# Kernel optimization log

Measured on AMD Instinct MI355X. Metric: run time of the kernel, lower is better.

## Reference

```python
import jax, jax.numpy as jnp
import numpy as np

N = 6144          # num utterances (graph nodes)
D = 128           # utt_embed_size
WIN = 10          # att_window_size
NUM_SPK = 8
N_EMO = 7


def _init(key, shape):
    fan_in = shape[0]
    return jax.random.normal(key, shape, dtype=jnp.float32) * (1.0 / np.sqrt(fan_in))


def setup_inputs() -> dict:
    key = jax.random.key(0)
    ks = jax.random.split(key, 20)
    inp = {
        "x": jax.random.normal(ks[0], (N, D), dtype=jnp.float32),
        "speakers": jax.random.randint(ks[1], (N,), 0, NUM_SPK, dtype=jnp.int32),
        # layer-1 relation GCN weights (pred / suc / same / diff)
        "W_pred1": _init(ks[2], (D, D)),
        "W_suc1": _init(ks[3], (D, D)),
        "W_same1": _init(ks[4], (D, D)),
        "W_diff1": _init(ks[5], (D, D)),
        # layer-2 relation GCN weights
        "W_pred2": _init(ks[6], (D, D)),
        "W_suc2": _init(ks[7], (D, D)),
        "W_same2": _init(ks[8], (D, D)),
        "W_diff2": _init(ks[9], (D, D)),
        "w_aggr_1": _init(ks[10], (D, D)),
        "w_aggr_2": _init(ks[11], (D, D)),
        "w_e1": _init(ks[12], (2 * D, D)),
        "b_e1": jnp.zeros((D,), dtype=jnp.float32),
        "w_e2": _init(ks[13], (D, N_EMO)),
        "b_e2": jnp.zeros((N_EMO,), dtype=jnp.float32),
        "w_s": _init(ks[14], (2 * D, N_EMO)),
        "b_s": jnp.zeros((N_EMO,), dtype=jnp.float32),
    }
    return inp


def reference(x, speakers, W_pred1, W_suc1, W_same1, W_diff1,
              W_pred2, W_suc2, W_same2, W_diff2,
              w_aggr_1, w_aggr_2, w_e1, b_e1, w_e2, b_e2, w_s, b_s):
    n = x.shape[0]
    idx = jnp.arange(n)
    # windowed dot-product attention; entries outside the window stay 0.0
    # BEFORE the softmax (faithful to the torch code: zeros, not -inf)
    band = jnp.abs(idx[:, None] - idx[None, :]) <= WIN
    scores = jnp.where(band, x @ x.T, 0.0)            # [N, N]
    attn = jax.nn.softmax(scores, axis=1)
    # relation masks
    same = (speakers[:, None] == speakers[None, :]).astype(x.dtype)
    pred = (idx[None, :] >= idx[:, None]).astype(x.dtype)   # triu incl diag
    suc = 1.0 - pred                                          # strict lower tri
    adjs = (same * pred * attn,        # same-speaker, predecessor
            same * suc * attn,         # same-speaker, successor
            (1.0 - same) * pred * attn,  # diff-speaker, predecessor
            (1.0 - same) * suc * attn)   # diff-speaker, successor

    def gcn(h, Ws):  # sum_k adj_k @ (h @ W_k)
        return sum(a @ (h @ w) for a, w in zip(adjs, Ws))

    d = jnp.diagonal(attn)[:, None]   # self-attention scale
    h1 = jax.nn.relu(gcn(x, (W_pred1, W_suc1, W_same1, W_diff1))
                     + (x @ w_aggr_1) * d)
    h2 = jax.nn.relu(gcn(h1, (W_pred2, W_suc2, W_same2, W_diff2))
                     + (h1 @ w_aggr_2) * d)
    h = jnp.concatenate([h2, x], axis=1)              # [N, 2D]
    emotion = jax.nn.relu(h @ w_e1 + b_e1) @ w_e2 + b_e2   # [N, 7]
    sentiment = h @ w_s + b_s                               # [N, 7]
    return emotion, sentiment
```

## Files before the change

kernel.cpp:

```cpp
#include <hip/hip_runtime.h>
#include <hip/hip_bf16.h>


#define NN   6144
#define DD   128
#define WINW 10
#define YST  168

typedef unsigned short u16;
typedef __attribute__((ext_vector_type(8))) short bf16x8;
typedef __attribute__((ext_vector_type(4))) float f32x4;

__device__ __forceinline__ float b2f(u16 u) {
    return __uint_as_float(((unsigned int)u) << 16);
}
__device__ __forceinline__ u16 f2b(float f) {
    __hip_bfloat16 h = __float2bfloat16(f);
    return *reinterpret_cast<u16*>(&h);
}
__device__ __forceinline__ bf16x8 cvt8(const float* p) {
    float4 u = *reinterpret_cast<const float4*>(p);
    float4 v = *reinterpret_cast<const float4*>(p + 4);
    bf16x8 r;
    r[0] = (short)f2b(u.x); r[1] = (short)f2b(u.y);
    r[2] = (short)f2b(u.z); r[3] = (short)f2b(u.w);
    r[4] = (short)f2b(v.x); r[5] = (short)f2b(v.y);
    r[6] = (short)f2b(v.z); r[7] = (short)f2b(v.w);
    return r;
}

__global__ __launch_bounds__(256) void prep_kernel(
    const float* __restrict__ x,
    const float* __restrict__ p0, const float* __restrict__ p1,
    const float* __restrict__ p2, const float* __restrict__ p3,
    const float* __restrict__ p4,
    const float* __restrict__ q0, const float* __restrict__ q1,
    const float* __restrict__ q2, const float* __restrict__ q3,
    const float* __restrict__ q4,
    const float* __restrict__ we1, const float* __restrict__ we2,
    const float* __restrict__ ws,
    u16* __restrict__ W1T, u16* __restrict__ W2T, u16* __restrict__ We1T,
    u16* __restrict__ we2T, u16* __restrict__ wsT,
    float* __restrict__ bandw)
{
    const int tid = threadIdx.x;

    if (blockIdx.x < 64) {
        int t = blockIdx.x * 256 + tid;
        const float* Ws1[5] = {p0, p1, p2, p3, p4};
        const float* Ws2[5] = {q0, q1, q2, q3, q4};
        #pragma unroll
        for (int r = 0; r < 5; ++r) {
            int idx = t + r * 16384;
            int k = idx & 127, c = (idx >> 7) & 127;
            W1T[idx] = f2b(Ws1[r][k * 128 + c]);
            W2T[idx] = f2b(Ws2[r][k * 128 + c]);
        }
        #pragma unroll
        for (int r = 0; r < 2; ++r) {
            int idx = t + r * 16384;
            int n = idx >> 8, k = idx & 255;
            We1T[idx] = f2b(we1[k * 128 + n]);
        }
        if (blockIdx.x == 0) {
            #pragma unroll
            for (int r = 0; r < 8; ++r) {
                int idx = tid + r * 256;
                int n = idx >> 7, k = idx & 127;
                we2T[idx] = f2b(n < 7 ? we2[k * 7 + n] : 0.f);
            }
            #pragma unroll
            for (int r = 0; r < 16; ++r) {
                int idx = tid + r * 256;
                int n = idx >> 8, k = idx & 255;
                wsT[idx] = f2b(n < 7 ? ws[k * 7 + n] : 0.f);
            }
        }
        return;
    }

    __shared__ float Xs[52][132];
    __shared__ float Ss[32][24];
    const int r0 = (blockIdx.x - 64) * 32;

    #pragma unroll
    for (int it = 0; it < 7; ++it) {
        int f = tid + it * 256;
        if (f < 52 * 32) {
            int s = f >> 5, c = f & 31;
            int g = r0 - WINW + s;
            if (g >= 0 && g < NN)
                *reinterpret_cast<float4*>(&Xs[s][c * 4]) =
                    *reinterpret_cast<const float4*>(&x[(size_t)g * DD + c * 4]);
        }
    }
    __syncthreads();

    #pragma unroll
    for (int r = 0; r < 3; ++r) {
        int p = tid + r * 256;
        if (p >= 672) break;
        int il = p / 21, o = p - il * 21;
        int jg = r0 + il - WINW + o;
        float sv = -1e30f;
        if (jg >= 0 && jg < NN) {
            const float* xr = &Xs[il + WINW][0];
            const float* jr = &Xs[il + o][0];
            float a0 = 0.f, a1 = 0.f, a2 = 0.f, a3 = 0.f;
            #pragma unroll 8
            for (int k4 = 0; k4 < 32; ++k4) {
                float4 a = *reinterpret_cast<const float4*>(xr + k4 * 4);
                float4 b = *reinterpret_cast<const float4*>(jr + k4 * 4);
                a0 = fmaf(a.x, b.x, a0); a1 = fmaf(a.y, b.y, a1);
                a2 = fmaf(a.z, b.z, a2); a3 = fmaf(a.w, b.w, a3);
            }
            sv = (a0 + a1) + (a2 + a3);
        }
        Ss[il][o] = sv;
    }
    __syncthreads();

    if (tid < 32) {
        int il = tid, i = r0 + il;
        float m = 0.f;
        #pragma unroll
        for (int o = 0; o < 21; ++o) {
            float s = Ss[il][o];
            if (s > -1e29f) m = fmaxf(m, s);
        }
        int lo = i - WINW; if (lo < 0) lo = 0;
        int hi = i + WINW; if (hi > NN - 1) hi = NN - 1;
        float Z = (float)(NN - (hi - lo + 1)) * expf(-m);
        float ev[21];
        #pragma unroll
        for (int o = 0; o < 21; ++o) {
            float s = Ss[il][o];
            ev[o] = (s > -1e29f) ? expf(s - m) : 0.f;
            Z += ev[o];
        }
        #pragma unroll
        for (int o = 0; o < 21; ++o) bandw[i * 32 + o] = ev[o] / Z;
    }
}

__global__ __launch_bounds__(256) void layer_kernel(
    const float* __restrict__ Af, const u16* __restrict__ Ab16,
    const u16* __restrict__ BT, const float* __restrict__ bandw,
    const int* __restrict__ spk, u16* __restrict__ hout, int a_is_f32)
{
    __shared__ u16 Ys[52][YST];
    __shared__ int2 tab[32 * 22];
    const int tid  = threadIdx.x;
    const int wave = tid >> 6, lane = tid & 63;
    const int lm = lane & 15, quad = lane >> 4;
    const int wm = wave >> 1, wn = wave & 1;
    const int bm = blockIdx.y * 32;
    const int hb = blockIdx.x;

    for (int p = tid; p < 704; p += 256) {
        int il = p / 22, e = p - il * 22;
        int i  = bm + il;
        int si = spk[i];
        float w; int off;
        if (e < 21) {
            int j = i - WINW + e;
            bool valid = (j >= 0) && (j < NN);
            int jc  = valid ? j : i;
            int sel = (spk[jc] == si) ? ((j >= i) ? 0 : 1) : ((j >= i) ? 2 : 3);
            w   = valid ? bandw[(size_t)i * 32 + e] : 0.f;
            off = valid ? (il + e) * YST + sel * 32 : 0;
        } else {
            w   = bandw[(size_t)i * 32 + WINW];
            off = (il + WINW) * YST + 4 * 32;
        }
        tab[p] = make_int2(__float_as_int(w), off);
    }

    bf16x8 afr[2][4];
    #pragma unroll
    for (int mt = 0; mt < 2; ++mt) {
        int gr = bm - WINW + (wm * 2 + mt) * 16 + lm;
        gr = min(max(gr, 0), NN - 1);
        #pragma unroll
        for (int s = 0; s < 4; ++s) {
            if (a_is_f32)
                afr[mt][s] = cvt8(Af + (size_t)gr * DD + s * 32 + quad * 8);
            else
                afr[mt][s] = *reinterpret_cast<const bf16x8*>(
                    Ab16 + (size_t)gr * DD + s * 32 + quad * 8);
        }
    }

    f32x4 acc[2][5];
    #pragma unroll
    for (int mt = 0; mt < 2; ++mt)
        #pragma unroll
        for (int n = 0; n < 5; ++n) acc[mt][n] = {0.f, 0.f, 0.f, 0.f};

    #pragma unroll
    for (int np = 0; np < 5; ++np) {
        int nt = wn * 5 + np;
        int gn = (nt >> 1) * 128 + hb * 32 + (nt & 1) * 16 + lm;
        #pragma unroll
        for (int s = 0; s < 4; ++s) {
            bf16x8 b = *reinterpret_cast<const bf16x8*>(
                BT + (size_t)gn * DD + s * 32 + quad * 8);
            acc[0][np] = __builtin_amdgcn_mfma_f32_16x16x32_bf16(afr[0][s], b, acc[0][np], 0, 0, 0);
            acc[1][np] = __builtin_amdgcn_mfma_f32_16x16x32_bf16(afr[1][s], b, acc[1][np], 0, 0, 0);
        }
    }
    #pragma unroll
    for (int mt = 0; mt < 2; ++mt)
        #pragma unroll
        for (int np = 0; np < 5; ++np) {
            int nt = wn * 5 + np;
            #pragma unroll
            for (int r = 0; r < 4; ++r) {
                int lr = (wm * 2 + mt) * 16 + quad * 4 + r;
                if (lr < 52) Ys[lr][nt * 16 + lm] = f2b(acc[mt][np][r]);
            }
        }
    __syncthreads();

    const int c0 = (tid & 15) * 2;
    const int rg = tid >> 4;
    #pragma unroll
    for (int rr = 0; rr < 2; ++rr) {
        int il = rg * 2 + rr;
        float a0 = 0.f, a1 = 0.f;
        const int2* tp = &tab[il * 22];
        #pragma unroll
        for (int e = 0; e < 22; ++e) {
            int2 t = tp[e];
            float w = __int_as_float(t.x);
            unsigned y2 = *reinterpret_cast<const unsigned*>(
                &Ys[0][0] + t.y + c0);
            a0 = fmaf(w, b2f((u16)(y2 & 0xffff)), a0);
            a1 = fmaf(w, b2f((u16)(y2 >> 16)), a1);
        }
        int i = bm + il;
        unsigned pk = ((unsigned)f2b(fmaxf(a1, 0.f)) << 16) | f2b(fmaxf(a0, 0.f));
        *reinterpret_cast<unsigned*>(&hout[(size_t)i * DD + hb * 32 + c0]) = pk;
    }
}

__global__ __launch_bounds__(64) void head_kernel(
    const u16* __restrict__ h2b, const float* __restrict__ x,
    const u16* __restrict__ We1T, const float* __restrict__ be1,
    const u16* __restrict__ we2T, const float* __restrict__ be2,
    const u16* __restrict__ wsT,  const float* __restrict__ bs,
    float* __restrict__ out)
{
    __shared__ float Es[16][132];
    const int lane = threadIdx.x;
    const int lm = lane & 15, quad = lane >> 4;
    const int bm = blockIdx.x * 16;
    const int row = bm + lm;

    bf16x8 afr[8];
    #pragma unroll
    for (int s = 0; s < 4; ++s)
        afr[s] = *reinterpret_cast<const bf16x8*>(
            &h2b[(size_t)row * DD + s * 32 + quad * 8]);
    #pragma unroll
    for (int s = 4; s < 8; ++s)
        afr[s] = cvt8(&x[(size_t)row * DD + (s - 4) * 32 + quad * 8]);

    f32x4 accE[8], accS = {0.f, 0.f, 0.f, 0.f};
    #pragma unroll
    for (int nt = 0; nt < 8; ++nt) accE[nt] = {0.f, 0.f, 0.f, 0.f};

    #pragma unroll
    for (int s = 0; s < 8; ++s) {
        #pragma unroll
        for (int nt = 0; nt < 8; ++nt) {
            bf16x8 b = *reinterpret_cast<const bf16x8*>(
                &We1T[(size_t)(nt * 16 + lm) * 256 + s * 32 + quad * 8]);
            accE[nt] = __builtin_amdgcn_mfma_f32_16x16x32_bf16(afr[s], b, accE[nt], 0, 0, 0);
        }
        bf16x8 bsf = *reinterpret_cast<const bf16x8*>(
            &wsT[(size_t)lm * 256 + s * 32 + quad * 8]);
        accS = __builtin_amdgcn_mfma_f32_16x16x32_bf16(afr[s], bsf, accS, 0, 0, 0);
    }

    if (lm < 7) {
        #pragma unroll
        for (int r = 0; r < 4; ++r) {
            int i = bm + quad * 4 + r;
            out[(size_t)NN * 7 + (size_t)i * 7 + lm] = accS[r] + bs[lm];
        }
    }
    #pragma unroll
    for (int nt = 0; nt < 8; ++nt) {
        int col = nt * 16 + lm;
        float bias = be1[col];
        #pragma unroll
        for (int r = 0; r < 4; ++r)
            Es[quad * 4 + r][col] = fmaxf(accE[nt][r] + bias, 0.f);
    }
    __syncthreads();

    f32x4 accM = {0.f, 0.f, 0.f, 0.f};
    #pragma unroll
    for (int s = 0; s < 4; ++s) {
        bf16x8 a = cvt8(&Es[lm][s * 32 + quad * 8]);
        bf16x8 b = *reinterpret_cast<const bf16x8*>(
            &we2T[(size_t)lm * 128 + s * 32 + quad * 8]);
        accM = __builtin_amdgcn_mfma_f32_16x16x32_bf16(a, b, accM, 0, 0, 0);
    }
    if (lm < 7) {
        #pragma unroll
        for (int r = 0; r < 4; ++r) {
            int i = bm + quad * 4 + r;
            out[(size_t)i * 7 + lm] = accM[r] + be2[lm];
        }
    }
}

extern "C" void kernel_launch(void* const* d_in, const int* in_sizes, int n_in,
                              void* d_out, int out_size, void* d_ws, size_t ws_size,
                              hipStream_t stream)
{
    const float* x   = (const float*)d_in[0];
    const int*   spk = (const int*)d_in[1];
    const float* Wp1 = (const float*)d_in[2];
    const float* Wu1 = (const float*)d_in[3];
    const float* Wm1 = (const float*)d_in[4];
    const float* Wd1 = (const float*)d_in[5];
    const float* Wp2 = (const float*)d_in[6];
    const float* Wu2 = (const float*)d_in[7];
    const float* Wm2 = (const float*)d_in[8];
    const float* Wd2 = (const float*)d_in[9];
    const float* wa1 = (const float*)d_in[10];
    const float* wa2 = (const float*)d_in[11];
    const float* we1 = (const float*)d_in[12];
    const float* be1 = (const float*)d_in[13];
    const float* we2 = (const float*)d_in[14];
    const float* be2 = (const float*)d_in[15];
    const float* wss = (const float*)d_in[16];
    const float* bss = (const float*)d_in[17];

    char* base = (char*)d_ws;
    float* bandw = (float*)(base);
    u16*   W1T   = (u16*)(base + 786432);
    u16*   W2T   = (u16*)(base + 950272);
    u16*   We1T  = (u16*)(base + 1114112);
    u16*   we2T  = (u16*)(base + 1179648);
    u16*   wsT   = (u16*)(base + 1183744);
    u16*   h1b   = (u16*)(base + 1191936);
    u16*   h2b   = (u16*)(base + 2764800);

    prep_kernel<<<256, 256, 0, stream>>>(x, Wp1, Wu1, Wm1, Wd1, wa1,
                                         Wp2, Wu2, Wm2, Wd2, wa2,
                                         we1, we2, wss,
                                         W1T, W2T, We1T, we2T, wsT, bandw);
    layer_kernel<<<dim3(4, 192), 256, 0, stream>>>(x, nullptr, W1T, bandw, spk, h1b, 1);
    layer_kernel<<<dim3(4, 192), 256, 0, stream>>>(nullptr, h1b, W2T, bandw, spk, h2b, 0);
    head_kernel<<<384, 64, 0, stream>>>(h2b, x, We1T, be1, we2T, be2, wsT, bss,
                                        (float*)d_out);
}
```

Baseline: 139.2 us.

## Increase block counts across prep, layer and head kernels for more parallelism

The attention-score blocks in the prep kernel now cover 16 rows instead of 32, so that section launches twice as many blocks. The layer kernel's column slice shrinks from 32 to 16 output columns, giving eight blocks per row tile, and each wave now owns one 16-row M tile. The head kernel uses 4 waves per block, splitting the E1 output tiles across waves and handing the sentiment and second-layer MFMAs to single waves. The goal is to fill more CUs on a small problem. The cost is recomputing the A fragments, the halo rows and the neighbour table in more blocks, plus idle waves in the head's tail.

Measured after the change: 158.5 us. +13.8%, slower.

```diff
diff --git a/kernel.cpp b/kernel.cpp
--- a/kernel.cpp
+++ b/kernel.cpp
@@ -5,7 +5,7 @@
 #define NN   6144
 #define DD   128
 #define WINW 10
-#define YST  168
+#define YST  88
 
 typedef unsigned short u16;
 typedef __attribute__((ext_vector_type(8))) short bf16x8;
@@ -79,14 +79,14 @@
         return;
     }
 
-    __shared__ float Xs[52][132];
-    __shared__ float Ss[32][24];
-    const int r0 = (blockIdx.x - 64) * 32;
-
-    #pragma unroll
-    for (int it = 0; it < 7; ++it) {
+    __shared__ float Xs[36][132];
+    __shared__ float Ss[16][24];
+    const int r0 = (blockIdx.x - 64) * 16;
+
+    #pragma unroll
+    for (int it = 0; it < 5; ++it) {
         int f = tid + it * 256;
-        if (f < 52 * 32) {
+        if (f < 36 * 32) {
             int s = f >> 5, c = f & 31;
             int g = r0 - WINW + s;
             if (g >= 0 && g < NN)
@@ -97,9 +97,9 @@
     __syncthreads();
 
     #pragma unroll
-    for (int r = 0; r < 3; ++r) {
+    for (int r = 0; r < 2; ++r) {
         int p = tid + r * 256;
-        if (p >= 672) break;
+        if (p >= 336) break;
         int il = p / 21, o = p - il * 21;
         int jg = r0 + il - WINW + o;
         float sv = -1e30f;
@@ -120,7 +120,7 @@
     }
     __syncthreads();
 
-    if (tid < 32) {
+    if (tid < 16) {
         int il = tid, i = r0 + il;
         float m = 0.f;
         #pragma unroll
@@ -153,7 +153,6 @@
     const int tid  = threadIdx.x;
     const int wave = tid >> 6, lane = tid & 63;
     const int lm = lane & 15, quad = lane >> 4;
-    const int wm = wave >> 1, wn = wave & 1;
     const int bm = blockIdx.y * 32;
     const int hb = blockIdx.x;
 
@@ -168,83 +167,67 @@
             int jc  = valid ? j : i;
             int sel = (spk[jc] == si) ? ((j >= i) ? 0 : 1) : ((j >= i) ? 2 : 3);
             w   = valid ? bandw[(size_t)i * 32 + e] : 0.f;
-            off = valid ? (il + e) * YST + sel * 32 : 0;
+            off = valid ? (il + e) * YST + sel * 16 : 0;
         } else {
             w   = bandw[(size_t)i * 32 + WINW];
-            off = (il + WINW) * YST + 4 * 32;
+            off = (il + WINW) * YST + 4 * 16;
         }
         tab[p] = make_int2(__float_as_int(w), off);
     }
 
-    bf16x8 afr[2][4];
-    #pragma unroll
-    for (int mt = 0; mt < 2; ++mt) {
-        int gr = bm - WINW + (wm * 2 + mt) * 16 + lm;
-        gr = min(max(gr, 0), NN - 1);
-        #pragma unroll
-        for (int s = 0; s < 4; ++s) {
-            if (a_is_f32)
-                afr[mt][s] = cvt8(Af + (size_t)gr * DD + s * 32 + quad * 8);
-            else
-                afr[mt][s] = *reinterpret_cast<const bf16x8*>(
-                    Ab16 + (size_t)gr * DD + s * 32 + quad * 8);
-        }
-    }
-
-    f32x4 acc[2][5];
-    #pragma unroll
-    for (int mt = 0; mt < 2; ++mt)
-        #pragma unroll
-        for (int n = 0; n < 5; ++n) acc[mt][n] = {0.f, 0.f, 0.f, 0.f};
-
-    #pragma unroll
-    for (int np = 0; np < 5; ++np) {
-        int nt = wn * 5 + np;
-        int gn = (nt >> 1) * 128 + hb * 32 + (nt & 1) * 16 + lm;
+    int gr = bm - WINW + wave * 16 + lm;
+    gr = min(max(gr, 0), NN - 1);
+    bf16x8 afr[4];
+    #pragma unroll
+    for (int s = 0; s < 4; ++s) {
+        if (a_is_f32)
+            afr[s] = cvt8(Af + (size_t)gr * DD + s * 32 + quad * 8);
+        else
+            afr[s] = *reinterpret_cast<const bf16x8*>(
+                Ab16 + (size_t)gr * DD + s * 32 + quad * 8);
+    }
+
+    f32x4 acc[5];
+    #pragma unroll
+    for (int n = 0; n < 5; ++n) acc[n] = {0.f, 0.f, 0.f, 0.f};
+
+    #pragma unroll
+    for (int nt = 0; nt < 5; ++nt) {
+        int gn = nt * 128 + hb * 16 + lm;
         #pragma unroll
         for (int s = 0; s < 4; ++s) {
             bf16x8 b = *reinterpret_cast<const bf16x8*>(
                 BT + (size_t)gn * DD + s * 32 + quad * 8);
-            acc[0][np] = __builtin_amdgcn_mfma_f32_16x16x32_bf16(afr[0][s], b, acc[0][np], 0, 0, 0);
-            acc[1][np] = __builtin_amdgcn_mfma_f32_16x16x32_bf16(afr[1][s], b, acc[1][np], 0, 0, 0);
-        }
-    }
-    #pragma unroll
-    for (int mt = 0; mt < 2; ++mt)
-        #pragma unroll
-        for (int np = 0; np < 5; ++np) {
-            int nt = wn * 5 + np;
-            #pragma unroll
-            for (int r = 0; r < 4; ++r) {
-                int lr = (wm * 2 + mt) * 16 + quad * 4 + r;
-                if (lr < 52) Ys[lr][nt * 16 + lm] = f2b(acc[mt][np][r]);
-            }
+            acc[nt] = __builtin_amdgcn_mfma_f32_16x16x32_bf16(afr[s], b, acc[nt], 0, 0, 0);
+        }
+    }
+    #pragma unroll
+    for (int nt = 0; nt < 5; ++nt)
+        #pragma unroll
+        for (int r = 0; r < 4; ++r) {
+            int lr = wave * 16 + quad * 4 + r;
+            if (lr < 52) Ys[lr][nt * 16 + lm] = f2b(acc[nt][r]);
         }
     __syncthreads();
 
-    const int c0 = (tid & 15) * 2;
-    const int rg = tid >> 4;
-    #pragma unroll
-    for (int rr = 0; rr < 2; ++rr) {
-        int il = rg * 2 + rr;
-        float a0 = 0.f, a1 = 0.f;
-        const int2* tp = &tab[il * 22];
-        #pragma unroll
-        for (int e = 0; e < 22; ++e) {
-            int2 t = tp[e];
-            float w = __int_as_float(t.x);
-            unsigned y2 = *reinterpret_cast<const unsigned*>(
-                &Ys[0][0] + t.y + c0);
-            a0 = fmaf(w, b2f((u16)(y2 & 0xffff)), a0);
-            a1 = fmaf(w, b2f((u16)(y2 >> 16)), a1);
-        }
-        int i = bm + il;
-        unsigned pk = ((unsigned)f2b(fmaxf(a1, 0.f)) << 16) | f2b(fmaxf(a0, 0.f));
-        *reinterpret_cast<unsigned*>(&hout[(size_t)i * DD + hb * 32 + c0]) = pk;
-    }
-}
-
-__global__ __launch_bounds__(64) void head_kernel(
+    const int c0 = (tid & 7) * 2;
+    const int il = tid >> 3;
+    float a0 = 0.f, a1 = 0.f;
+    const int2* tp = &tab[il * 22];
+    #pragma unroll
+    for (int e = 0; e < 22; ++e) {
+        int2 t = tp[e];
+        float w = __int_as_float(t.x);
+        unsigned y2 = *reinterpret_cast<const unsigned*>(&Ys[0][0] + t.y + c0);
+        a0 = fmaf(w, b2f((u16)(y2 & 0xffff)), a0);
+        a1 = fmaf(w, b2f((u16)(y2 >> 16)), a1);
+    }
+    int i = bm + il;
+    unsigned pk = ((unsigned)f2b(fmaxf(a1, 0.f)) << 16) | f2b(fmaxf(a0, 0.f));
+    *reinterpret_cast<unsigned*>(&hout[(size_t)i * DD + hb * 16 + c0]) = pk;
+}
+
+__global__ __launch_bounds__(256) void head_kernel(
     const u16* __restrict__ h2b, const float* __restrict__ x,
     const u16* __restrict__ We1T, const float* __restrict__ be1,
     const u16* __restrict__ we2T, const float* __restrict__ be2,
@@ -252,7 +235,8 @@
     float* __restrict__ out)
 {
     __shared__ float Es[16][132];
-    const int lane = threadIdx.x;
+    const int tid  = threadIdx.x;
+    const int wave = tid >> 6, lane = tid & 63;
     const int lm = lane & 15, quad = lane >> 4;
     const int bm = blockIdx.x * 16;
     const int row = bm + lm;
@@ -266,24 +250,27 @@
     for (int s = 4; s < 8; ++s)
         afr[s] = cvt8(&x[(size_t)row * DD + (s - 4) * 32 + quad * 8]);
 
-    f32x4 accE[8], accS = {0.f, 0.f, 0.f, 0.f};
-    #pragma unroll
-    for (int nt = 0; nt < 8; ++nt) accE[nt] = {0.f, 0.f, 0.f, 0.f};
+    f32x4 accE[2], accS = {0.f, 0.f, 0.f, 0.f};
+    accE[0] = {0.f, 0.f, 0.f, 0.f};
+    accE[1] = {0.f, 0.f, 0.f, 0.f};
 
     #pragma unroll
     for (int s = 0; s < 8; ++s) {
         #pragma unroll
-        for (int nt = 0; nt < 8; ++nt) {
+        for (int t = 0; t < 2; ++t) {
+            int nt = wave * 2 + t;
             bf16x8 b = *reinterpret_cast<const bf16x8*>(
                 &We1T[(size_t)(nt * 16 + lm) * 256 + s * 32 + quad * 8]);
-            accE[nt] = __builtin_amdgcn_mfma_f32_16x16x32_bf16(afr[s], b, accE[nt], 0, 0, 0);
-        }
-        bf16x8 bsf = *reinterpret_cast<const bf16x8*>(
-            &wsT[(size_t)lm * 256 + s * 32 + quad * 8]);
-        accS = __builtin_amdgcn_mfma_f32_16x16x32_bf16(afr[s], bsf, accS, 0, 0, 0);
-    }
-
-    if (lm < 7) {
+            accE[t] = __builtin_amdgcn_mfma_f32_16x16x32_bf16(afr[s], b, accE[t], 0, 0, 0);
+        }
+        if (wave == 3) {
+            bf16x8 bsf = *reinterpret_cast<const bf16x8*>(
+                &wsT[(size_t)lm * 256 + s * 32 + quad * 8]);
+            accS = __builtin_amdgcn_mfma_f32_16x16x32_bf16(afr[s], bsf, accS, 0, 0, 0);
+        }
+    }
+
+    if (wave == 3 && lm < 7) {
         #pragma unroll
         for (int r = 0; r < 4; ++r) {
             int i = bm + quad * 4 + r;
@@ -291,28 +278,30 @@
         }
     }
     #pragma unroll
-    for (int nt = 0; nt < 8; ++nt) {
-        int col = nt * 16 + lm;
+    for (int t = 0; t < 2; ++t) {
+        int col = (wave * 2 + t) * 16 + lm;
         float bias = be1[col];
         #pragma unroll
         for (int r = 0; r < 4; ++r)
-            Es[quad * 4 + r][col] = fmaxf(accE[nt][r] + bias, 0.f);
+            Es[quad * 4 + r][col] = fmaxf(accE[t][r] + bias, 0.f);
     }
     __syncthreads();
 
-    f32x4 accM = {0.f, 0.f, 0.f, 0.f};
-    #pragma unroll
-    for (int s = 0; s < 4; ++s) {
-        bf16x8 a = cvt8(&Es[lm][s * 32 + quad * 8]);
-        bf16x8 b = *reinterpret_cast<const bf16x8*>(
-            &we2T[(size_t)lm * 128 + s * 32 + quad * 8]);
-        accM = __builtin_amdgcn_mfma_f32_16x16x32_bf16(a, b, accM, 0, 0, 0);
-    }
-    if (lm < 7) {
-        #pragma unroll
-        for (int r = 0; r < 4; ++r) {
-            int i = bm + quad * 4 + r;
-            out[(size_t)i * 7 + lm] = accM[r] + be2[lm];
+    if (wave == 0) {
+        f32x4 accM = {0.f, 0.f, 0.f, 0.f};
+        #pragma unroll
+        for (int s = 0; s < 4; ++s) {
+            bf16x8 a = cvt8(&Es[lm][s * 32 + quad * 8]);
+            bf16x8 b = *reinterpret_cast<const bf16x8*>(
+                &we2T[(size_t)lm * 128 + s * 32 + quad * 8]);
+            accM = __builtin_amdgcn_mfma_f32_16x16x32_bf16(a, b, accM, 0, 0, 0);
+        }
+        if (lm < 7) {
+            #pragma unroll
+            for (int r = 0; r < 4; ++r) {
+                int i = bm + quad * 4 + r;
+                out[(size_t)i * 7 + lm] = accM[r] + be2[lm];
+            }
         }
     }
 }
@@ -350,12 +339,12 @@
     u16*   h1b   = (u16*)(base + 1191936);
     u16*   h2b   = (u16*)(base + 2764800);
 
-    prep_kernel<<<256, 256, 0, stream>>>(x, Wp1, Wu1, Wm1, Wd1, wa1,
+    prep_kernel<<<448, 256, 0, stream>>>(x, Wp1, Wu1, Wm1, Wd1, wa1,
                                          Wp2, Wu2, Wm2, Wd2, wa2,
                                          we1, we2, wss,
                                          W1T, W2T, We1T, we2T, wsT, bandw);
-    layer_kernel<<<dim3(4, 192), 256, 0, stream>>>(x, nullptr, W1T, bandw, spk, h1b, 1);
-    layer_kernel<<<dim3(4, 192), 256, 0, stream>>>(nullptr, h1b, W2T, bandw, spk, h2b, 0);
-    head_kernel<<<384, 64, 0, stream>>>(h2b, x, We1T, be1, we2T, be2, wsT, bss,
-                                        (float*)d_out);
-}
+    layer_kernel<<<dim3(8, 192), 256, 0, stream>>>(x, nullptr, W1T, bandw, spk, h1b, 1);
+    layer_kernel<<<dim3(8, 192), 256, 0, stream>>>(nullptr, h1b, W2T, bandw, spk, h2b, 0);
+    head_kernel<<<384, 256, 0, stream>>>(h2b, x, We1T, be1, we2T, be2, wsT, bss,
+                                         (float*)d_out);
+}
```
